# Kernel tuning notes

Measured on AMD Instinct MI355X. Metric: run time of the kernel, lower is better.

The kernel has to match this reference:

```python
import jax, jax.numpy as jnp
import numpy as np

B, T, I, H = 1024, 64, 64, 1024
FUTURE = 16


def lstm_cell(x_t, h, c, Wih, Whh, b_ih, b_hh):
    # torch LSTMCell gate order: i, f, g, o; weights are (4H, in)
    gates = x_t @ Wih.T + h @ Whh.T + b_ih + b_hh  # (B, 4H)
    i, f, g, o = jnp.split(gates, 4, axis=-1)
    i = jax.nn.sigmoid(i)
    f = jax.nn.sigmoid(f)
    g = jnp.tanh(g)
    o = jax.nn.sigmoid(o)
    c_new = f * c + i * g
    h_new = o * jnp.tanh(c_new)
    return h_new, c_new


def setup_inputs() -> dict:
    key = jax.random.key(0)
    ks = jax.random.split(key, 12)
    s1 = 1.0 / np.sqrt(H)
    inp = {
        "x": jax.random.normal(ks[0], (B, T, I), dtype=jnp.float32),
        "W_ih1": jax.random.uniform(ks[1], (4 * H, I), jnp.float32, -s1, s1),
        "W_hh1": jax.random.uniform(ks[2], (4 * H, H), jnp.float32, -s1, s1),
        "b_ih1": jax.random.uniform(ks[3], (4 * H,), jnp.float32, -s1, s1),
        "b_hh1": jax.random.uniform(ks[4], (4 * H,), jnp.float32, -s1, s1),
        "W_ih2": jax.random.uniform(ks[5], (4 * H, H), jnp.float32, -s1, s1),
        "W_hh2": jax.random.uniform(ks[6], (4 * H, H), jnp.float32, -s1, s1),
        "b_ih2": jax.random.uniform(ks[7], (4 * H,), jnp.float32, -s1, s1),
        "b_hh2": jax.random.uniform(ks[8], (4 * H,), jnp.float32, -s1, s1),
        "W_lin": jax.random.uniform(ks[9], (I, H), jnp.float32, -s1, s1),
        "b_lin": jax.random.uniform(ks[10], (I,), jnp.float32, -s1, s1),
        "future": FUTURE,
    }
    return inp


def reference(x, W_ih1, W_hh1, b_ih1, b_hh1, W_ih2, W_hh2, b_ih2, b_hh2,
              W_lin, b_lin, future):
    b_size = x.shape[0]
    zeros = jnp.zeros((b_size, H), dtype=x.dtype)

    def two_layer_step(h1, c1, h2, c2, x_t):
        h1, c1 = lstm_cell(x_t, h1, c1, W_ih1, W_hh1, b_ih1, b_hh1)
        h2, c2 = lstm_cell(h1, h2, c2, W_ih2, W_hh2, b_ih2, b_hh2)
        out = h2 @ W_lin.T + b_lin  # (B, I)
        return h1, c1, h2, c2, out

    def step(carry, x_t):
        h1, c1, h2, c2 = carry
        h1, c1, h2, c2, out = two_layer_step(h1, c1, h2, c2, x_t)
        return (h1, c1, h2, c2), out

    xs = jnp.transpose(x, (1, 0, 2))  # (T, B, I)
    carry, outs = jax.lax.scan(step, (zeros, zeros, zeros, zeros), xs)

    if future > 0:
        def fstep(carry, _):
            h1, c1, h2, c2, out = carry
            h1, c1, h2, c2, out = two_layer_step(h1, c1, h2, c2, out)
            return (h1, c1, h2, c2, out), out

        h1, c1, h2, c2 = carry
        _, fouts = jax.lax.scan(fstep, (h1, c1, h2, c2, outs[-1]),
                                None, length=future)
        outs = jnp.concatenate([outs, fouts], axis=0)

    return jnp.transpose(outs, (1, 0, 2))  # (B, T+future, I)
```

## Files before the change

### kernel.cpp

```cpp
#include <hip/hip_runtime.h>


#define B_   1024
#define T_   64
#define I_   64
#define H_   1024
#define FUT_ 16
#define NST_ (T_ + FUT_)
#define SROW 2176

typedef _Float16 half8_t  __attribute__((ext_vector_type(8)));
typedef float    float4_t __attribute__((ext_vector_type(4)));

typedef __attribute__((address_space(1))) const unsigned int g_u32;
typedef __attribute__((address_space(3))) unsigned int l_u32;

__device__ __forceinline__ void load_lds16(const _Float16* g, _Float16* l) {
    __builtin_amdgcn_global_load_lds((g_u32*)g, (l_u32*)l, 16, 0, 0);
}

__device__ __forceinline__ float sigmoid_f(float x) {
    x = fminf(fmaxf(x, -30.f), 30.f);
    return __fdividef(1.f, 1.f + __expf(-x));
}
__device__ __forceinline__ float tanh_f(float x) {
    x = fminf(fmaxf(x, -15.f), 15.f);
    float e = __expf(2.f * x);
    return 1.f - 2.f * __fdividef(1.f, e + 1.f);
}

__global__ void convert_all(const float* __restrict__ x,
    const float* __restrict__ Wih1, const float* __restrict__ Whh1,
    const float* __restrict__ bih1, const float* __restrict__ bhh1,
    const float* __restrict__ Wih2, const float* __restrict__ Whh2,
    const float* __restrict__ bih2, const float* __restrict__ bhh2,
    const float* __restrict__ Wlin,
    _Float16* __restrict__ W1p, _Float16* __restrict__ W2p,
    _Float16* __restrict__ Wlp,
    _Float16* __restrict__ S0x, _Float16* __restrict__ S1x,
    float* __restrict__ b1, float* __restrict__ b2)
{
    size_t idx = (size_t)blockIdx.x * 256 + threadIdx.x;
    const size_t nc1 = 589824;
    const size_t nc2 = 1048576;
    const size_t nc3 = 8192;
    const size_t nx  = 65536;
    if (idx < nc1) {
        int c = (int)idx;
        int lane = c & 63, g = (c >> 6) & 3, rem = c >> 8;
        int j = rem % 36, hgrp = rem / 36;
        int row = (g << 10) + hgrp * 16 + (lane & 15);
        int kb = j * 32 + (lane >> 4) * 8;
        _Float16* o = &W1p[(size_t)c * 8];
        if (kb < 1024) {
            #pragma unroll
            for (int i = 0; i < 8; ++i) o[i] = (_Float16)Whh1[(size_t)row * 1024 + kb + i];
        } else if (kb < 1088) {
            #pragma unroll
            for (int i = 0; i < 8; ++i) o[i] = (_Float16)Wih1[row * 64 + (kb - 1024) + i];
        } else {
            #pragma unroll
            for (int i = 0; i < 8; ++i) o[i] = (_Float16)0.f;
        }
    } else if ((idx -= nc1) < nc2) {
        int c = (int)idx;
        int lane = c & 63, g = (c >> 6) & 3, rem = c >> 8;
        int j = rem & 63, hgrp = rem >> 6;
        int row = (g << 10) + hgrp * 16 + (lane & 15);
        int kb = j * 32 + (lane >> 4) * 8;
        _Float16* o = &W2p[(size_t)c * 8];
        if (kb < 1024) {
            #pragma unroll
            for (int i = 0; i < 8; ++i) o[i] = (_Float16)Wih2[(size_t)row * 1024 + kb + i];
        } else {
            #pragma unroll
            for (int i = 0; i < 8; ++i) o[i] = (_Float16)Whh2[(size_t)row * 1024 + kb - 1024 + i];
        }
    } else if ((idx -= nc2) < nc3) {
        int c = (int)idx;
        int lane = c & 63, j = (c >> 6) & 31, hgrp = c >> 11;
        int row = hgrp * 16 + (lane & 15);
        int kb = j * 32 + (lane >> 4) * 8;
        _Float16* o = &Wlp[(size_t)c * 8];
        #pragma unroll
        for (int i = 0; i < 8; ++i) o[i] = (_Float16)Wlin[(size_t)row * 1024 + kb + i];
    } else if ((idx -= nc3) < nx) {
        int b = (int)(idx >> 6), i = (int)(idx & 63);
        S0x[(size_t)b * SROW + i] = (_Float16)x[(size_t)b * (T_ * I_) + i];
    } else if ((idx -= nx) < nx) {
        int b = (int)(idx >> 6), i = (int)(idx & 63);
        S1x[(size_t)b * SROW + i] = (_Float16)x[(size_t)b * (T_ * I_) + 64 + i];
    } else if ((idx -= nx) < 4096) {
        b1[idx] = bih1[idx] + bhh1[idx];
    } else if ((idx -= 4096) < 4096) {
        b2[idx] = bih2[idx] + bhh2[idx];
    }
}

__global__ void compose_pack(const float* __restrict__ Wih1,
    const float* __restrict__ Whh1, const float* __restrict__ Wlin,
    const float* __restrict__ blin, const float* __restrict__ b1in,
    _Float16* __restrict__ W1c2, float* __restrict__ bc1)
{
    size_t idx = (size_t)blockIdx.x * 256 + threadIdx.x;
    const size_t NC = 1048576;
    if (idx < NC) {
        int c = (int)idx;
        int lane = c & 63, g = (c >> 6) & 3, rem = c >> 8;
        int j = rem & 63, hgrp = rem >> 6;
        int row = (g << 10) + hgrp * 16 + (lane & 15);
        int kb = j * 32 + (lane >> 4) * 8;
        _Float16* o = &W1c2[(size_t)c * 8];
        if (kb < 1024) {
            #pragma unroll
            for (int i = 0; i < 8; ++i) o[i] = (_Float16)Whh1[(size_t)row * 1024 + kb + i];
        } else {
            const int h = kb - 1024;
            float acc[8] = {0, 0, 0, 0, 0, 0, 0, 0};
            for (int i2 = 0; i2 < 64; ++i2) {
                float wv = Wih1[row * 64 + i2];
                const float* wl = &Wlin[(size_t)i2 * 1024 + h];
                #pragma unroll
                for (int e = 0; e < 8; ++e) acc[e] += wv * wl[e];
            }
            #pragma unroll
            for (int e = 0; e < 8; ++e) o[e] = (_Float16)acc[e];
        }
    } else if ((idx -= NC) < 4096) {
        int n = (int)idx;
        float s = b1in[n];
        for (int i2 = 0; i2 < 64; ++i2) s += Wih1[n * 64 + i2] * blin[i2];
        bc1[n] = s;
    }
}

__device__ __forceinline__ void gemm_body(_Float16* sAb,
    const _Float16* __restrict__ Alo, const _Float16* __restrict__ Ahi,
    const _Float16* __restrict__ Wp, const int iters, const int Ksh,
    const float* __restrict__ bias, float* __restrict__ cvec,
    _Float16* __restrict__ hdst, const int unit)
{
    const int tid = threadIdx.x;
    const int lane = tid & 63, w = tid >> 6;
    const int hw = w & 1, kh = w >> 1;
    const int lr = lane & 15, lq = lane >> 4;
    const int ht = ((unit & 7) << 2) | ((unit >> 3) & 3);
    const int mt = unit >> 5;
    const int h0 = ht * 32, m0 = mt * 64;
    const int hgrp = ht * 2 + hw;

    const char* wptr = (const char*)Wp
        + ((size_t)hgrp * (2 * Ksh) + (size_t)kh * Ksh) * 4096
        + (size_t)lane * 16;

    const int srow0 = tid >> 4, pg = tid & 15;
    const int gg = pg ^ (srow0 & 15);
    const _Float16* asrc = (gg < 8 ? Alo : Ahi) + (gg & 7) * 8
                         + (size_t)(m0 + srow0) * SROW;

    const int ag0 = ((kh * 8 + lq) ^ lr) * 8;
    const int ag1 = ((kh * 8 + 4 + lq) ^ lr) * 8;

    float4_t acc[4][4];
    #pragma unroll
    for (int g = 0; g < 4; ++g)
        #pragma unroll
        for (int rt = 0; rt < 4; ++rt)
            #pragma unroll
            for (int e = 0; e < 4; ++e) acc[g][rt][e] = 0.f;

    half8_t bfc[8], bfn[8];
    #pragma unroll
    for (int q = 0; q < 8; ++q)
        bfc[q] = *(const half8_t*)(wptr + q * 1024);

    #pragma unroll
    for (int s = 0; s < 4; ++s)
        load_lds16(asrc + (size_t)s * 16 * SROW, sAb + tid * 8 + s * 2048);

    for (int i = 0; i < iters; ++i) {
        __syncthreads();
        _Float16* cur = sAb + (i & 1) * 8192;
        if (i + 1 < iters) {
            _Float16* nxt = sAb + ((i + 1) & 1) * 8192;
            const _Float16* an = asrc + (size_t)(i + 1) * 64;
            #pragma unroll
            for (int s = 0; s < 4; ++s)
                load_lds16(an + (size_t)s * 16 * SROW, nxt + tid * 8 + s * 2048);
            const char* wn = wptr + 8192;
            #pragma unroll
            for (int q = 0; q < 8; ++q)
                bfn[q] = *(const half8_t*)(wn + q * 1024);
        }
        #pragma unroll
        for (int ks = 0; ks < 2; ++ks) {
            const int ag = ks ? ag1 : ag0;
            #pragma unroll
            for (int rt = 0; rt < 4; ++rt) {
                half8_t af = *(const half8_t*)&cur[(rt * 16 + lr) * 128 + ag];
                #pragma unroll
                for (int g = 0; g < 4; ++g)
                    acc[g][rt] = __builtin_amdgcn_mfma_f32_16x16x32_f16(
                        af, bfc[ks * 4 + g], acc[g][rt], 0, 0, 0);
            }
        }
        wptr += 8192;
        #pragma unroll
        for (int q = 0; q < 8; ++q) bfc[q] = bfn[q];
    }
    __syncthreads();

    float* scr = (float*)sAb;
    #pragma unroll
    for (int gp = 0; gp < 2; ++gp) {
        if (kh == 1) {
            #pragma unroll
            for (int g2 = 0; g2 < 2; ++g2)
                #pragma unroll
                for (int rt = 0; rt < 4; ++rt) {
                    int slot = ((hw * 2 + g2) * 4 + rt) * 64 + lane;
                    *(float4_t*)&scr[slot * 4] = acc[gp * 2 + g2][rt];
                }
        }
        __syncthreads();
        if (kh == 0) {
            #pragma unroll
            for (int g2 = 0; g2 < 2; ++g2)
                #pragma unroll
                for (int rt = 0; rt < 4; ++rt) {
                    int slot = ((hw * 2 + g2) * 4 + rt) * 64 + lane;
                    acc[gp * 2 + g2][rt] += *(const float4_t*)&scr[slot * 4];
                }
        }
        __syncthreads();
    }
    if (kh != 0) return;

    const int j = h0 + hw * 16 + lr;
    const float bi = bias[j], bff = bias[1024 + j];
    const float bg = bias[2048 + j], bo = bias[3072 + j];
    #pragma unroll
    for (int rt = 0; rt < 4; ++rt) {
        #pragma unroll
        for (int e = 0; e < 4; ++e) {
            const int brow = m0 + rt * 16 + lq * 4 + e;
            float gi = sigmoid_f(acc[0][rt][e] + bi);
            float gf = sigmoid_f(acc[1][rt][e] + bff);
            float gv = tanh_f(acc[2][rt][e] + bg);
            float go = sigmoid_f(acc[3][rt][e] + bo);
            const size_t ci = (size_t)brow * 1024 + j;
            float cn = gf * cvec[ci] + gi * gv;
            cvec[ci] = cn;
            hdst[(size_t)brow * SROW + j] = (_Float16)(go * tanh_f(cn));
        }
    }
}

__device__ __forceinline__ void proj_body(_Float16* sA,
    const _Float16* __restrict__ A, const _Float16* __restrict__ Wp,
    const float* __restrict__ blin, float* __restrict__ outp,
    const int unit)
{
    const int iters = 8;
    const int tid = threadIdx.x;
    const int lane = tid & 63, w = tid >> 6;
    const int hw = w & 1, kh = w >> 1;
    const int lr = lane & 15, lq = lane >> 4;
    const int ht = unit & 1, mt = unit >> 1;
    const int h0 = ht * 32, m0 = mt * 64;
    const int hgrp = ht * 2 + hw;

    const char* wptr = (const char*)Wp
        + ((size_t)hgrp * 32 + (size_t)kh * 16) * 1024 + (size_t)lane * 16;

    const int srow0 = tid >> 4, pg = tid & 15;
    const int gg = pg ^ (srow0 & 15);
    const _Float16* asrc = A + (size_t)(gg >> 3) * 512 + (gg & 7) * 8
                         + (size_t)(m0 + srow0) * SROW;
    _Float16* ldst = sA + tid * 8;
    const int ag0 = ((kh * 8 + lq) ^ lr) * 8;
    const int ag1 = ((kh * 8 + 4 + lq) ^ lr) * 8;

    float4_t acc[4];
    #pragma unroll
    for (int rt = 0; rt < 4; ++rt)
        #pragma unroll
        for (int e = 0; e < 4; ++e) acc[rt][e] = 0.f;

    half8_t b0 = *(const half8_t*)(wptr);
    half8_t b1v = *(const half8_t*)(wptr + 1024);
    for (int i = 0; i < iters; ++i) {
        #pragma unroll
        for (int s = 0; s < 4; ++s)
            load_lds16(asrc + (size_t)s * 16 * SROW + (size_t)i * 64,
                       ldst + s * 2048);
        __syncthreads();
        half8_t n0, n1;
        if (i + 1 < iters) {
            n0 = *(const half8_t*)(wptr + 2048);
            n1 = *(const half8_t*)(wptr + 3072);
        }
        half8_t af;
        #pragma unroll
        for (int rt = 0; rt < 4; ++rt) {
            af = *(const half8_t*)&sA[(rt * 16 + lr) * 128 + ag0];
            acc[rt] = __builtin_amdgcn_mfma_f32_16x16x32_f16(af, b0, acc[rt], 0, 0, 0);
        }
        #pragma unroll
        for (int rt = 0; rt < 4; ++rt) {
            af = *(const half8_t*)&sA[(rt * 16 + lr) * 128 + ag1];
            acc[rt] = __builtin_amdgcn_mfma_f32_16x16x32_f16(af, b1v, acc[rt], 0, 0, 0);
        }
        __syncthreads();
        wptr += 2048;
        b0 = n0; b1v = n1;
    }

    float* scr = (float*)sA;
    if (kh == 1) {
        #pragma unroll
        for (int rt = 0; rt < 4; ++rt) {
            int slot = (hw * 4 + rt) * 64 + lane;
            *(float4_t*)&scr[slot * 4] = acc[rt];
        }
    }
    __syncthreads();
    if (kh != 0) return;
    #pragma unroll
    for (int rt = 0; rt < 4; ++rt) {
        int slot = (hw * 4 + rt) * 64 + lane;
        acc[rt] += *(const float4_t*)&scr[slot * 4];
    }

    const int j = h0 + hw * 16 + lr;
    const float bj = blin[j];
    #pragma unroll
    for (int rt = 0; rt < 4; ++rt) {
        #pragma unroll
        for (int e = 0; e < 4; ++e) {
            const int brow = m0 + rt * 16 + lq * 4 + e;
            outp[(size_t)brow * (NST_ * I_) + j] = acc[rt][e] + bj;
        }
    }
}

struct StepArgs {
    int nL2, nL1, nProj, nCopy;
    const _Float16 *l2Alo, *l2Ahi; _Float16* l2H; const float* l2b; float* c2;
    const _Float16 *l1Alo, *l1Ahi; _Float16* l1H; const float* l1b; float* c1;
    int l1Iters, l1Ksh; const _Float16* l1W;
    const _Float16* pA; float* pOut;
    const float* xsrc; _Float16* xdst;
    const _Float16 *W2p, *Wlp;
    const float* blin;
};

__global__ __launch_bounds__(256, 3) void fused_step(StepArgs a) {
    __shared__ __align__(16) _Float16 sA[16384];
    int bid = blockIdx.x;
    if (bid < a.nL2) {
        gemm_body(sA, a.l2Alo, a.l2Ahi, a.W2p, 16, 32, a.l2b, a.c2, a.l2H, bid);
    } else if ((bid -= a.nL2) < a.nL1) {
        gemm_body(sA, a.l1Alo, a.l1Ahi, a.l1W, a.l1Iters, a.l1Ksh,
                  a.l1b, a.c1, a.l1H, bid);
    } else if ((bid -= a.nL1) < a.nProj) {
        proj_body(sA, a.pA, a.Wlp, a.blin, a.pOut, bid);
    } else {
        bid -= a.nProj;
        int base = bid * 256 + threadIdx.x;
        for (int k = base; k < B_ * I_; k += a.nCopy * 256) {
            int b = k >> 6, i = k & 63;
            a.xdst[(size_t)b * SROW + i] = (_Float16)a.xsrc[(size_t)b * (T_ * I_) + i];
        }
    }
}

extern "C" void kernel_launch(void* const* d_in, const int* in_sizes, int n_in,
                              void* d_out, int out_size, void* d_ws, size_t ws_size,
                              hipStream_t stream) {
    (void)in_sizes; (void)n_in; (void)out_size; (void)ws_size;
    const float* x    = (const float*)d_in[0];
    const float* Wih1 = (const float*)d_in[1];
    const float* Whh1 = (const float*)d_in[2];
    const float* bih1 = (const float*)d_in[3];
    const float* bhh1 = (const float*)d_in[4];
    const float* Wih2 = (const float*)d_in[5];
    const float* Whh2 = (const float*)d_in[6];
    const float* bih2 = (const float*)d_in[7];
    const float* bhh2 = (const float*)d_in[8];
    const float* Wlin = (const float*)d_in[9];
    const float* blin = (const float*)d_in[10];
    float* out = (float*)d_out;

    char* p = (char*)d_ws;
    auto alloc = [&](size_t bytes) {
        char* r = p; p += (bytes + 255) & ~(size_t)255; return r;
    };
    _Float16* W1p  = (_Float16*)alloc((size_t)4096 * 1152 * 2);
    _Float16* W2p  = (_Float16*)alloc((size_t)4096 * 2048 * 2);
    _Float16* W1c2 = (_Float16*)alloc((size_t)4096 * 2048 * 2);
    _Float16* Wlp  = (_Float16*)alloc((size_t)64 * 1024 * 2);
    _Float16* S[3];
    for (int i = 0; i < 3; ++i) S[i] = (_Float16*)alloc((size_t)B_ * SROW * 2);
    float* c1  = (float*)alloc((size_t)B_ * H_ * 4);
    float* c2  = (float*)alloc((size_t)B_ * H_ * 4);
    float* b1  = (float*)alloc(4096 * 4);
    float* b2  = (float*)alloc(4096 * 4);
    float* bc1 = (float*)alloc(4096 * 4);

    for (int i = 0; i < 3; ++i)
        hipMemsetAsync(S[i], 0, (size_t)B_ * SROW * 2, stream);
    hipMemsetAsync(c1, 0, (size_t)B_ * H_ * 4, stream);
    hipMemsetAsync(c2, 0, (size_t)B_ * H_ * 4, stream);

    {
        const size_t total = 589824 + 1048576 + 8192 + 65536 + 65536 + 8192;
        convert_all<<<(int)((total + 255) / 256), 256, 0, stream>>>(
            x, Wih1, Whh1, bih1, bhh1, Wih2, Whh2, bih2, bhh2, Wlin,
            W1p, W2p, Wlp, S[0] + 1024, S[1] + 1024, b1, b2);
        compose_pack<<<(int)((1048576 + 4096 + 255) / 256), 256, 0, stream>>>(
            Wih1, Whh1, Wlin, blin, b1, W1c2, bc1);
    }

    StepArgs a{};
    a.W2p = W2p; a.Wlp = Wlp; a.blin = blin;
    a.l2b = b2; a.c2 = c2; a.l1b = b1; a.c1 = c1;
    a.l1W = W1p; a.l1Iters = 9; a.l1Ksh = 18;

    {
        StepArgs q = a;
        q.nL2 = 0; q.nL1 = 512; q.nProj = 0; q.nCopy = 0;
        q.l1Alo = S[0]; q.l1Ahi = S[0] + 576; q.l1H = S[1];
        fused_step<<<512, 256, 0, stream>>>(q);
    }

    for (int t = 0; t <= 62; ++t) {
        _Float16* Sp = S[t % 3];
        _Float16* Sq = S[(t + 1) % 3];
        _Float16* Sn = S[(t + 2) % 3];
        StepArgs q = a;
        q.nL2 = 512; q.nL1 = 512;
        q.nProj = (t >= 1) ? 32 : 0;
        q.nCopy = (t <= 61) ? 16 : 0;
        q.l2Alo = Sq; q.l2Ahi = Sp + 1152; q.l2H = Sq + 1152;
        q.l1Alo = Sq; q.l1Ahi = Sq + 576; q.l1H = Sn;
        q.pA = Sp + 1152; q.pOut = out + (size_t)(t - 1) * I_;
        q.xsrc = x + (size_t)(t + 2) * I_; q.xdst = Sn + 1024;
        int grid = q.nL2 + q.nL1 + q.nProj + q.nCopy;
        fused_step<<<grid, 256, 0, stream>>>(q);
    }

    {
        StepArgs q = a;
        q.nL2 = 512; q.nL1 = 0; q.nProj = 32; q.nCopy = 0;
        q.l2Alo = S[1]; q.l2Ahi = S[0] + 1152; q.l2H = S[1] + 1152;
        q.pA = S[0] + 1152; q.pOut = out + (size_t)62 * I_;
        fused_step<<<544, 256, 0, stream>>>(q);
    }

    for (int t = T_; t < NST_; ++t) {
        _Float16* Sp = S[1 + ((t - T_) & 1)];
        _Float16* Sq = S[1 + (((t - T_) & 1) ^ 1)];
        {
            StepArgs q = a;
            q.nL2 = 0; q.nL1 = 512; q.nProj = 32; q.nCopy = 0;
            q.l1W = W1c2; q.l1Iters = 16; q.l1Ksh = 32; q.l1b = bc1;
            q.l1Alo = Sp; q.l1Ahi = Sp + 1152; q.l1H = Sq;
            q.pA = Sp + 1152; q.pOut = out + (size_t)(t - 1) * I_;
            fused_step<<<544, 256, 0, stream>>>(q);
        }
        {
            StepArgs q = a;
            q.nL2 = 512; q.nL1 = 0; q.nProj = 0; q.nCopy = 0;
            q.l2Alo = Sq; q.l2Ahi = Sp + 1152; q.l2H = Sq + 1152;
            fused_step<<<512, 256, 0, stream>>>(q);
        }
    }

    {
        _Float16* Sl = S[1 + (((NST_ - 1 - T_) & 1) ^ 1)];
        StepArgs q = a;
        q.nL2 = 0; q.nL1 = 0; q.nProj = 32; q.nCopy = 0;
        q.pA = Sl + 1152; q.pOut = out + (size_t)(NST_ - 1) * I_;
        fused_step<<<32, 256, 0, stream>>>(q);
    }
}
```

Before: 3.561 ms.

## Load GEMM A operands directly to registers and tile the composed-weight precompute

The recurrent GEMM body stops staging the activation tile through LDS with global_load_lds and double-buffered __syncthreads. Each wave now loads its own A fragments straight from global memory into double-buffered registers, with the iteration count as a template parameter so the loop fully unrolls. LDS is kept only for the cross-wave K reduction, and launch bounds drop from 3 to 2 blocks per SM. Separately, the composed Wih1·Wlin weight precompute becomes a shared-memory tiled GEMM, and the Whh1 copy into W1c2 moves into the conversion kernel. The trade is removing LDS sync and staging in exchange for redundant global loads across waves, higher register pressure and lower occupancy.

```diff
diff --git a/kernel.cpp b/kernel.cpp
--- a/kernel.cpp
+++ b/kernel.cpp
@@ -36,15 +36,16 @@
     const float* __restrict__ bih2, const float* __restrict__ bhh2,
     const float* __restrict__ Wlin,
     _Float16* __restrict__ W1p, _Float16* __restrict__ W2p,
-    _Float16* __restrict__ Wlp,
+    _Float16* __restrict__ W1c2, _Float16* __restrict__ Wlp,
     _Float16* __restrict__ S0x, _Float16* __restrict__ S1x,
     float* __restrict__ b1, float* __restrict__ b2)
 {
     size_t idx = (size_t)blockIdx.x * 256 + threadIdx.x;
-    const size_t nc1 = 589824;
-    const size_t nc2 = 1048576;
-    const size_t nc3 = 8192;
-    const size_t nx  = 65536;
+    const size_t nc1  = 589824;
+    const size_t nc2  = 1048576;
+    const size_t nc2b = 524288;
+    const size_t nc3  = 8192;
+    const size_t nx   = 65536;
     if (idx < nc1) {
         int c = (int)idx;
         int lane = c & 63, g = (c >> 6) & 3, rem = c >> 8;
@@ -76,7 +77,16 @@
             #pragma unroll
             for (int i = 0; i < 8; ++i) o[i] = (_Float16)Whh2[(size_t)row * 1024 + kb - 1024 + i];
         }
-    } else if ((idx -= nc2) < nc3) {
+    } else if ((idx -= nc2) < nc2b) {
+        int c = (int)idx;
+        int lane = c & 63, g = (c >> 6) & 3, rem = c >> 8;
+        int j = rem & 31, hgrp = rem >> 5;
+        int row = (g << 10) + hgrp * 16 + (lane & 15);
+        int kb = j * 32 + (lane >> 4) * 8;
+        _Float16* o = &W1c2[((((size_t)hgrp * 64 + j) * 4 + g) * 512) + lane * 8];
+        #pragma unroll
+        for (int i = 0; i < 8; ++i) o[i] = (_Float16)Whh1[(size_t)row * 1024 + kb + i];
+    } else if ((idx -= nc2b) < nc3) {
         int c = (int)idx;
         int lane = c & 63, j = (c >> 6) & 31, hgrp = c >> 11;
         int row = hgrp * 16 + (lane & 15);
@@ -97,49 +107,63 @@
     }
 }
 
-__global__ void compose_pack(const float* __restrict__ Wih1,
-    const float* __restrict__ Whh1, const float* __restrict__ Wlin,
+__global__ __launch_bounds__(256) void compose_tile(
+    const float* __restrict__ Wih1, const float* __restrict__ Wlin,
     const float* __restrict__ blin, const float* __restrict__ b1in,
     _Float16* __restrict__ W1c2, float* __restrict__ bc1)
 {
-    size_t idx = (size_t)blockIdx.x * 256 + threadIdx.x;
-    const size_t NC = 1048576;
-    if (idx < NC) {
-        int c = (int)idx;
-        int lane = c & 63, g = (c >> 6) & 3, rem = c >> 8;
-        int j = rem & 63, hgrp = rem >> 6;
-        int row = (g << 10) + hgrp * 16 + (lane & 15);
-        int kb = j * 32 + (lane >> 4) * 8;
-        _Float16* o = &W1c2[(size_t)c * 8];
-        if (kb < 1024) {
-            #pragma unroll
-            for (int i = 0; i < 8; ++i) o[i] = (_Float16)Whh1[(size_t)row * 1024 + kb + i];
-        } else {
-            const int h = kb - 1024;
-            float acc[8] = {0, 0, 0, 0, 0, 0, 0, 0};
-            for (int i2 = 0; i2 < 64; ++i2) {
-                float wv = Wih1[row * 64 + i2];
-                const float* wl = &Wlin[(size_t)i2 * 1024 + h];
-                #pragma unroll
-                for (int e = 0; e < 8; ++e) acc[e] += wv * wl[e];
-            }
-            #pragma unroll
-            for (int e = 0; e < 8; ++e) o[e] = (_Float16)acc[e];
-        }
-    } else if ((idx -= NC) < 4096) {
-        int n = (int)idx;
+    if (blockIdx.x >= 1024) {
+        int n = (blockIdx.x - 1024) * 256 + threadIdx.x;
         float s = b1in[n];
-        for (int i2 = 0; i2 < 64; ++i2) s += Wih1[n * 64 + i2] * blin[i2];
+        for (int i = 0; i < 64; ++i) s += Wih1[n * 64 + i] * blin[i];
         bc1[n] = s;
-    }
-}
-
-__device__ __forceinline__ void gemm_body(_Float16* sAb,
+        return;
+    }
+    __shared__ float sa[64][68];
+    __shared__ float swl[64][68];
+    const int tid = threadIdx.x;
+    const int r0 = (blockIdx.x >> 4) * 64, c0 = (blockIdx.x & 15) * 64;
+    #pragma unroll
+    for (int t = 0; t < 16; ++t) {
+        int e = tid + t * 256;
+        int rr = e >> 6, cc = e & 63;
+        sa[rr][cc]  = Wih1[(size_t)(r0 + rr) * 64 + cc];
+        swl[rr][cc] = Wlin[(size_t)rr * 1024 + c0 + cc];
+    }
+    __syncthreads();
+    const int tr = (tid >> 3) * 2, tc = (tid & 7) * 8;
+    float acc[2][8] = {};
+    for (int k = 0; k < 64; ++k) {
+        float a0 = sa[tr][k], a1 = sa[tr + 1][k];
+        #pragma unroll
+        for (int j = 0; j < 8; ++j) {
+            float wv = swl[k][tc + j];
+            acc[0][j] += a0 * wv;
+            acc[1][j] += a1 * wv;
+        }
+    }
+    #pragma unroll
+    for (int rr = 0; rr < 2; ++rr) {
+        const int row = r0 + tr + rr;
+        const int g = row >> 10, hgrp = (row & 1023) >> 4, lr16 = row & 15;
+        const int hcol = c0 + tc;
+        const int j = 32 + (hcol >> 5), lq = (hcol >> 3) & 3;
+        half8_t v;
+        #pragma unroll
+        for (int e2 = 0; e2 < 8; ++e2) v[e2] = (_Float16)acc[rr][e2];
+        *(half8_t*)(W1c2 + ((((size_t)hgrp * 64 + j) * 4 + g) * 512
+                    + (lq * 16 + lr16) * 8)) = v;
+    }
+}
+
+template<int ITERS>
+__device__ __forceinline__ void gemm_body(float* scr,
     const _Float16* __restrict__ Alo, const _Float16* __restrict__ Ahi,
-    const _Float16* __restrict__ Wp, const int iters, const int Ksh,
+    const _Float16* __restrict__ Wp,
     const float* __restrict__ bias, float* __restrict__ cvec,
     _Float16* __restrict__ hdst, const int unit)
 {
+    constexpr int KSH = 2 * ITERS;
     const int tid = threadIdx.x;
     const int lane = tid & 63, w = tid >> 6;
     const int hw = w & 1, kh = w >> 1;
@@ -150,16 +174,9 @@
     const int hgrp = ht * 2 + hw;
 
     const char* wptr = (const char*)Wp
-        + ((size_t)hgrp * (2 * Ksh) + (size_t)kh * Ksh) * 4096
-        + (size_t)lane * 16;
-
-    const int srow0 = tid >> 4, pg = tid & 15;
-    const int gg = pg ^ (srow0 & 15);
-    const _Float16* asrc = (gg < 8 ? Alo : Ahi) + (gg & 7) * 8
-                         + (size_t)(m0 + srow0) * SROW;
-
-    const int ag0 = ((kh * 8 + lq) ^ lr) * 8;
-    const int ag1 = ((kh * 8 + 4 + lq) ^ lr) * 8;
+        + ((size_t)hgrp * (2 * KSH) + (size_t)kh * KSH) * 4096;
+    const _Float16* aptr0 = (kh ? Ahi : Alo)
+        + (size_t)(m0 + lr) * SROW + lq * 8;
 
     float4_t acc[4][4];
     #pragma unroll
@@ -169,50 +186,45 @@
             #pragma unroll
             for (int e = 0; e < 4; ++e) acc[g][rt][e] = 0.f;
 
-    half8_t bfc[8], bfn[8];
+    half8_t af[2][2][4], bf[2][8];
+    #pragma unroll
+    for (int ks = 0; ks < 2; ++ks)
+        #pragma unroll
+        for (int rt = 0; rt < 4; ++rt)
+            af[0][ks][rt] = *(const half8_t*)(aptr0
+                + (size_t)rt * 16 * SROW + ks * 32);
     #pragma unroll
     for (int q = 0; q < 8; ++q)
-        bfc[q] = *(const half8_t*)(wptr + q * 1024);
-
-    #pragma unroll
-    for (int s = 0; s < 4; ++s)
-        load_lds16(asrc + (size_t)s * 16 * SROW, sAb + tid * 8 + s * 2048);
-
-    for (int i = 0; i < iters; ++i) {
-        __syncthreads();
-        _Float16* cur = sAb + (i & 1) * 8192;
-        if (i + 1 < iters) {
-            _Float16* nxt = sAb + ((i + 1) & 1) * 8192;
-            const _Float16* an = asrc + (size_t)(i + 1) * 64;
-            #pragma unroll
-            for (int s = 0; s < 4; ++s)
-                load_lds16(an + (size_t)s * 16 * SROW, nxt + tid * 8 + s * 2048);
-            const char* wn = wptr + 8192;
+        bf[0][q] = *(const half8_t*)(wptr + q * 1024 + lane * 16);
+
+    #pragma unroll
+    for (int i = 0; i < ITERS; ++i) {
+        const int cur = i & 1, nxt = cur ^ 1;
+        if (i + 1 < ITERS) {
+            #pragma unroll
+            for (int ks = 0; ks < 2; ++ks)
+                #pragma unroll
+                for (int rt = 0; rt < 4; ++rt)
+                    af[nxt][ks][rt] = *(const half8_t*)(aptr0
+                        + (size_t)rt * 16 * SROW + (i + 1) * 64 + ks * 32);
             #pragma unroll
             for (int q = 0; q < 8; ++q)
-                bfn[q] = *(const half8_t*)(wn + q * 1024);
-        }
-        #pragma unroll
-        for (int ks = 0; ks < 2; ++ks) {
-            const int ag = ks ? ag1 : ag0;
-            #pragma unroll
-            for (int rt = 0; rt < 4; ++rt) {
-                half8_t af = *(const half8_t*)&cur[(rt * 16 + lr) * 128 + ag];
+                bf[nxt][q] = *(const half8_t*)(wptr
+                    + (size_t)(i + 1) * 8192 + q * 1024 + lane * 16);
+        }
+        #pragma unroll
+        for (int ks = 0; ks < 2; ++ks)
+            #pragma unroll
+            for (int rt = 0; rt < 4; ++rt)
                 #pragma unroll
                 for (int g = 0; g < 4; ++g)
                     acc[g][rt] = __builtin_amdgcn_mfma_f32_16x16x32_f16(
-                        af, bfc[ks * 4 + g], acc[g][rt], 0, 0, 0);
-            }
-        }
-        wptr += 8192;
-        #pragma unroll
-        for (int q = 0; q < 8; ++q) bfc[q] = bfn[q];
-    }
-    __syncthreads();
-
-    float* scr = (float*)sAb;
+                        af[cur][ks][rt], bf[cur][ks * 4 + g], acc[g][rt], 0, 0, 0);
+    }
+
     #pragma unroll
     for (int gp = 0; gp < 2; ++gp) {
+        __syncthreads();
         if (kh == 1) {
             #pragma unroll
             for (int g2 = 0; g2 < 2; ++g2)
@@ -232,7 +244,6 @@
                     acc[gp * 2 + g2][rt] += *(const float4_t*)&scr[slot * 4];
                 }
         }
-        __syncthreads();
     }
     if (kh != 0) return;
 
@@ -345,26 +356,32 @@
 }
 
 struct StepArgs {
-    int nL2, nL1, nProj, nCopy;
-    const _Float16 *l2Alo, *l2Ahi; _Float16* l2H; const float* l2b; float* c2;
-    const _Float16 *l1Alo, *l1Ahi; _Float16* l1H; const float* l1b; float* c1;
-    int l1Iters, l1Ksh; const _Float16* l1W;
+    int nL2, nL1, nProj, nCopy, l1Mode;
+    const _Float16 *l2Alo, *l2Ahi; _Float16* l2H;
+    const _Float16 *l1Alo, *l1Ahi; _Float16* l1H;
+    const _Float16* l1W; const float* l1b;
     const _Float16* pA; float* pOut;
     const float* xsrc; _Float16* xdst;
     const _Float16 *W2p, *Wlp;
-    const float* blin;
+    const float *b2, *blin;
+    float *c1, *c2;
 };
 
-__global__ __launch_bounds__(256, 3) void fused_step(StepArgs a) {
-    __shared__ __align__(16) _Float16 sA[16384];
+__global__ __launch_bounds__(256, 2) void fused_step(StepArgs a) {
+    __shared__ __align__(16) char smem[16384];
     int bid = blockIdx.x;
     if (bid < a.nL2) {
-        gemm_body(sA, a.l2Alo, a.l2Ahi, a.W2p, 16, 32, a.l2b, a.c2, a.l2H, bid);
+        gemm_body<16>((float*)smem, a.l2Alo, a.l2Ahi, a.W2p,
+                      a.b2, a.c2, a.l2H, bid);
     } else if ((bid -= a.nL2) < a.nL1) {
-        gemm_body(sA, a.l1Alo, a.l1Ahi, a.l1W, a.l1Iters, a.l1Ksh,
-                  a.l1b, a.c1, a.l1H, bid);
+        if (a.l1Mode)
+            gemm_body<16>((float*)smem, a.l1Alo, a.l1Ahi, a.l1W,
+                          a.l1b, a.c1, a.l1H, bid);
+        else
+            gemm_body<9>((float*)smem, a.l1Alo, a.l1Ahi, a.l1W,
+                         a.l1b, a.c1, a.l1H, bid);
     } else if ((bid -= a.nL1) < a.nProj) {
-        proj_body(sA, a.pA, a.Wlp, a.blin, a.pOut, bid);
+        proj_body((_Float16*)smem, a.pA, a.Wlp, a.blin, a.pOut, bid);
     } else {
         bid -= a.nProj;
         int base = bid * 256 + threadIdx.x;
@@ -414,18 +431,18 @@
     hipMemsetAsync(c2, 0, (size_t)B_ * H_ * 4, stream);
 
     {
-        const size_t total = 589824 + 1048576 + 8192 + 65536 + 65536 + 8192;
+        const size_t total = 589824 + 1048576 + 524288 + 8192
+                           + 65536 + 65536 + 8192;
         convert_all<<<(int)((total + 255) / 256), 256, 0, stream>>>(
             x, Wih1, Whh1, bih1, bhh1, Wih2, Whh2, bih2, bhh2, Wlin,
-            W1p, W2p, Wlp, S[0] + 1024, S[1] + 1024, b1, b2);
-        compose_pack<<<(int)((1048576 + 4096 + 255) / 256), 256, 0, stream>>>(
-            Wih1, Whh1, Wlin, blin, b1, W1c2, bc1);
+            W1p, W2p, W1c2, Wlp, S[0] + 1024, S[1] + 1024, b1, b2);
+        compose_tile<<<1040, 256, 0, stream>>>(Wih1, Wlin, blin, b1, W1c2, bc1);
     }
 
     StepArgs a{};
     a.W2p = W2p; a.Wlp = Wlp; a.blin = blin;
-    a.l2b = b2; a.c2 = c2; a.l1b = b1; a.c1 = c1;
-    a.l1W = W1p; a.l1Iters = 9; a.l1Ksh = 18;
+    a.b2 = b2; a.c1 = c1; a.c2 = c2;
+    a.l1W = W1p; a.l1b = b1; a.l1Mode = 0;
 
     {
         StepArgs q = a;
@@ -464,7 +481,7 @@
         {
             StepArgs q = a;
             q.nL2 = 0; q.nL1 = 512; q.nProj = 32; q.nCopy = 0;
-            q.l1W = W1c2; q.l1Iters = 16; q.l1Ksh = 32; q.l1b = bc1;
+            q.l1Mode = 1; q.l1W = W1c2; q.l1b = bc1;
             q.l1Alo = Sp; q.l1Ahi = Sp + 1152; q.l1H = Sq;
             q.pA = Sp + 1152; q.pOut = out + (size_t)(t - 1) * I_;
             fused_step<<<544, 256, 0, stream>>>(q);
```

After: 5.950 ms. 1.67x slower.
